# Kernel tuning notes

Measured on AMD Instinct MI355X. Metric: run time of the kernel, lower is better.

## Reference

```python
import jax, jax.numpy as jnp
import numpy as np


def setup_inputs() -> dict:
    key = jax.random.key(0)
    x = jax.random.normal(key, (8, 64, 512, 512), dtype=jnp.float32)
    return {"x": x}


def reference(x):
    # Haar wavelet via strided 2x2 pixel blocks (equivalent to the per-channel
    # conv2d with the LL/LH/HL/HH 2x2 filter bank, stride 2, no padding).
    # Block layout: [[a, b], [c, d]] with a at (even row, even col).
    a = x[:, :, 0::2, 0::2]
    b = x[:, :, 0::2, 1::2]
    c = x[:, :, 1::2, 0::2]
    d = x[:, :, 1::2, 1::2]
    half = jnp.asarray(0.5, x.dtype)
    ll = (a + b + c + d) * half           # LL = [[1,1],[1,1]]/2 (cross-correlation)
    lh = (-a - b + c + d) * half          # LH = [[-1,-1],[1,1]]/2
    hl = (-a + b - c + d) * half          # HL = [[-1,1],[-1,1]]/2
    hh = (a - b - c + d) * half           # HH = [[1,-1],[-1,1]]/2
    low = ll
    high = lh + hl + hh
    return (low, high)
```

## Files before the change

kernel.cpp:

```cpp
#include <hip/hip_runtime.h>


__global__ __launch_bounds__(256) void haar_kernel(
    const float* __restrict__ x,
    float* __restrict__ low,
    float* __restrict__ high,
    unsigned n_items)
{
    unsigned idx = blockIdx.x * blockDim.x + threadIdx.x;
    const unsigned stride = gridDim.x * blockDim.x;
    for (; idx < n_items; idx += stride) {
        const unsigned jp = idx & 127u;
        const unsigned i  = (idx >> 7) & 255u;
        const unsigned p  = idx >> 15;

        const unsigned in_base = p * 262144u + (2u * i) * 512u + 4u * jp;
        const float4 v0 = *reinterpret_cast<const float4*>(x + in_base);
        const float4 v1 = *reinterpret_cast<const float4*>(x + in_base + 512u);

        const float a0 = v0.x, b0 = v0.y, a1 = v0.z, b1 = v0.w;
        const float c0 = v1.x, d0 = v1.y, c1 = v1.z, d1 = v1.w;

        const float lo0 = 0.5f * (a0 + b0 + c0 + d0);
        const float lo1 = 0.5f * (a1 + b1 + c1 + d1);
        const float hi0 = 0.5f * (3.0f * d0 - a0 - b0 - c0);
        const float hi1 = 0.5f * (3.0f * d1 - a1 - b1 - c1);

        const unsigned obase = p * 65536u + i * 256u + 2u * jp;
        *reinterpret_cast<float2*>(low + obase)  = make_float2(lo0, lo1);
        *reinterpret_cast<float2*>(high + obase) = make_float2(hi0, hi1);
    }
}

extern "C" void kernel_launch(void* const* d_in, const int* in_sizes, int n_in,
                              void* d_out, int out_size, void* d_ws, size_t ws_size,
                              hipStream_t stream) {
    const float* x = (const float*)d_in[0];
    float* out = (float*)d_out;

    const unsigned half = (unsigned)(out_size / 2);
    float* low  = out;
    float* high = out + half;

    const unsigned n_items = half / 2;
    const int block = 256;
    const int grid = 2048;

    haar_kernel<<<grid, block, 0, stream>>>(x, low, high, n_items);
}
```

Before: 167.2 us.

## Process one output row per wavefront with shuffled 16-byte stores and nontemporal access

Each wavefront now handles one full output row: it loads two float4 per input row per lane, computes four outputs, then uses cross-lane shuffles so each lane writes a float4 to low and high. Loads and stores are nontemporal, and the grid-stride loop is replaced by one work item per thread over a 32768-block grid. The aim is to widen stores from 8 to 16 bytes and cut cache pollution in this bandwidth-bound kernel. In exchange it adds 16 shuffles per thread and hardcodes the problem size into the grid.

Result: faster. 134.7 us (-19.4%).

```diff
diff --git a/kernel.cpp b/kernel.cpp
--- a/kernel.cpp
+++ b/kernel.cpp
@@ -1,35 +1,53 @@
 #include <hip/hip_runtime.h>
 
+
+typedef float f32x4 __attribute__((ext_vector_type(4)));
 
 __global__ __launch_bounds__(256) void haar_kernel(
     const float* __restrict__ x,
     float* __restrict__ low,
-    float* __restrict__ high,
-    unsigned n_items)
+    float* __restrict__ high)
 {
-    unsigned idx = blockIdx.x * blockDim.x + threadIdx.x;
-    const unsigned stride = gridDim.x * blockDim.x;
-    for (; idx < n_items; idx += stride) {
-        const unsigned jp = idx & 127u;
-        const unsigned i  = (idx >> 7) & 255u;
-        const unsigned p  = idx >> 15;
+    const unsigned lane = threadIdx.x & 63u;
+    const unsigned wid  = (blockIdx.x << 2) | (threadIdx.x >> 6);
+    const unsigned p = wid >> 8;
+    const unsigned i = wid & 255u;
 
-        const unsigned in_base = p * 262144u + (2u * i) * 512u + 4u * jp;
-        const float4 v0 = *reinterpret_cast<const float4*>(x + in_base);
-        const float4 v1 = *reinterpret_cast<const float4*>(x + in_base + 512u);
+    const float* row0 = x + p * 262144u + (2u * i) * 512u;
+    const f32x4* r0 = reinterpret_cast<const f32x4*>(row0);
+    const f32x4* r1 = reinterpret_cast<const f32x4*>(row0 + 512);
 
-        const float a0 = v0.x, b0 = v0.y, a1 = v0.z, b1 = v0.w;
-        const float c0 = v1.x, d0 = v1.y, c1 = v1.z, d1 = v1.w;
+    const f32x4 va0 = __builtin_nontemporal_load(r0 + lane);
+    const f32x4 va1 = __builtin_nontemporal_load(r0 + 64 + lane);
+    const f32x4 vb0 = __builtin_nontemporal_load(r1 + lane);
+    const f32x4 vb1 = __builtin_nontemporal_load(r1 + 64 + lane);
 
-        const float lo0 = 0.5f * (a0 + b0 + c0 + d0);
-        const float lo1 = 0.5f * (a1 + b1 + c1 + d1);
-        const float hi0 = 0.5f * (3.0f * d0 - a0 - b0 - c0);
-        const float hi1 = 0.5f * (3.0f * d1 - a1 - b1 - c1);
+    const float loA0 = 0.5f * (va0.x + va0.y + vb0.x + vb0.y);
+    const float hiA0 = 0.5f * (3.0f * vb0.y - va0.x - va0.y - vb0.x);
+    const float loA1 = 0.5f * (va0.z + va0.w + vb0.z + vb0.w);
+    const float hiA1 = 0.5f * (3.0f * vb0.w - va0.z - va0.w - vb0.z);
+    const float loB0 = 0.5f * (va1.x + va1.y + vb1.x + vb1.y);
+    const float hiB0 = 0.5f * (3.0f * vb1.y - va1.x - va1.y - vb1.x);
+    const float loB1 = 0.5f * (va1.z + va1.w + vb1.z + vb1.w);
+    const float hiB1 = 0.5f * (3.0f * vb1.w - va1.z - va1.w - vb1.z);
 
-        const unsigned obase = p * 65536u + i * 256u + 2u * jp;
-        *reinterpret_cast<float2*>(low + obase)  = make_float2(lo0, lo1);
-        *reinterpret_cast<float2*>(high + obase) = make_float2(hi0, hi1);
-    }
+    const int s0 = (int)((2u * lane) & 63u);
+    const int s1 = s0 + 1;
+    const bool first = lane < 32u;
+
+    f32x4 lo4, hi4;
+    { const float a = __shfl(loA0, s0), b = __shfl(loB0, s0); lo4.x = first ? a : b; }
+    { const float a = __shfl(loA1, s0), b = __shfl(loB1, s0); lo4.y = first ? a : b; }
+    { const float a = __shfl(loA0, s1), b = __shfl(loB0, s1); lo4.z = first ? a : b; }
+    { const float a = __shfl(loA1, s1), b = __shfl(loB1, s1); lo4.w = first ? a : b; }
+    { const float a = __shfl(hiA0, s0), b = __shfl(hiB0, s0); hi4.x = first ? a : b; }
+    { const float a = __shfl(hiA1, s0), b = __shfl(hiB1, s0); hi4.y = first ? a : b; }
+    { const float a = __shfl(hiA0, s1), b = __shfl(hiB0, s1); hi4.z = first ? a : b; }
+    { const float a = __shfl(hiA1, s1), b = __shfl(hiB1, s1); hi4.w = first ? a : b; }
+
+    const unsigned obase = p * 65536u + i * 256u + 4u * lane;
+    __builtin_nontemporal_store(lo4, reinterpret_cast<f32x4*>(low + obase));
+    __builtin_nontemporal_store(hi4, reinterpret_cast<f32x4*>(high + obase));
 }
 
 extern "C" void kernel_launch(void* const* d_in, const int* in_sizes, int n_in,
@@ -42,9 +60,8 @@
     float* low  = out;
     float* high = out + half;
 
-    const unsigned n_items = half / 2;
     const int block = 256;
-    const int grid = 2048;
+    const int grid = 32768;
 
-    haar_kernel<<<grid, block, 0, stream>>>(x, low, high, n_items);
+    haar_kernel<<<grid, block, 0, stream>>>(x, low, high);
 }
```
